# Kernel optimization log

Hardware: AMD Instinct MI355X
Metric: run time of the kernel (lower is better)

## Reference

```python
import jax, jax.numpy as jnp
import numpy as np


def setup_inputs() -> dict:
    key = jax.random.key(0)
    k1, k2, k3 = jax.random.split(key, 3)
    N, D, E = 100000, 128, 600000
    h = jax.random.normal(k1, (N, D), dtype=jnp.float32)
    src = jax.random.randint(k2, (E,), 0, N, dtype=jnp.int64)
    dst = jax.random.randint(k3, (E,), 0, N, dtype=jnp.int64)
    return {"h": h, "src": src, "dst": dst}


def reference(h, src, dst):
    # DGL fn.u_dot_v('h','h','out'): per-edge dot product of src/dst node
    # features, output shape (E, 1).
    hu = h[src]            # (E, D) gather of source-node features
    hv = h[dst]            # (E, D) gather of destination-node features
    out = jnp.sum(hu * hv, axis=-1, keepdims=True)  # (E, 1)
    return out
```

## Files before the change

kernel.cpp:

```cpp
#include <hip/hip_runtime.h>
#include <hip/hip_fp16.h>


constexpr int D   = 128;
constexpr int LPE = 16;
constexpr int UNR = 4;

__global__ __launch_bounds__(256) void convert_kernel(
    const float* __restrict__ h, __half* __restrict__ hh, int n4)
{
    const int stride = gridDim.x * blockDim.x;
    for (int k = blockIdx.x * blockDim.x + threadIdx.x; k < n4; k += stride) {
        float4 v = reinterpret_cast<const float4*>(h)[k];
        __half2 a = __floats2half2_rn(v.x, v.y);
        __half2 b = __floats2half2_rn(v.z, v.w);
        uint2 packed;
        packed.x = *reinterpret_cast<unsigned int*>(&a);
        packed.y = *reinterpret_cast<unsigned int*>(&b);
        reinterpret_cast<uint2*>(hh)[k] = packed;
    }
}

#if defined(__has_builtin) && __has_builtin(__builtin_amdgcn_fdot2)
#define HAS_FDOT2 1
#else
#define HAS_FDOT2 0
#endif

__device__ __forceinline__ float dot8(uint4 ua, uint4 ub)
{
    float acc = 0.f;
    const unsigned int* pa = &ua.x;
    const unsigned int* pb = &ub.x;
#pragma unroll
    for (int i = 0; i < 4; ++i) {
        __half2 ha = *reinterpret_cast<const __half2*>(&pa[i]);
        __half2 hb = *reinterpret_cast<const __half2*>(&pb[i]);
#if HAS_FDOT2
        acc = __builtin_amdgcn_fdot2(*reinterpret_cast<_Float16_2*>(&ha),
                                     *reinterpret_cast<_Float16_2*>(&hb),
                                     acc, false);
#else
        float2 fa = __half22float2(ha);
        float2 fb = __half22float2(hb);
        acc = fmaf(fa.x, fb.x, acc);
        acc = fmaf(fa.y, fb.y, acc);
#endif
    }
    return acc;
}

__device__ __forceinline__ float reduce16(float acc)
{
    acc += __shfl_xor(acc, 1);
    acc += __shfl_xor(acc, 2);
    acc += __shfl_xor(acc, 4);
    acc += __shfl_xor(acc, 8);
    return acc;
}

__global__ __launch_bounds__(256) void edge_dot_f16_kernel(
    const __half* __restrict__ hh,
    const int*    __restrict__ src,
    const int*    __restrict__ dst,
    float*        __restrict__ out,
    int E)
{
    const int tid    = blockIdx.x * blockDim.x + threadIdx.x;
    const int sub    = threadIdx.x & (LPE - 1);
    const int slot   = tid / LPE;
    const int nslots = (gridDim.x * blockDim.x) / LPE;
    const int step   = UNR * nslots;

    int e = slot;
    int s[UNR], t[UNR];
    if (e + (UNR - 1) * nslots < E) {
#pragma unroll
        for (int k = 0; k < UNR; ++k) {
            s[k] = src[e + k * nslots];
            t[k] = dst[e + k * nslots];
        }
    }

    while (e + (UNR - 1) * nslots < E) {
        uint4 a[UNR], b[UNR];
#pragma unroll
        for (int k = 0; k < UNR; ++k) {
            a[k] = *(reinterpret_cast<const uint4*>(hh + (size_t)s[k] * D) + sub);
            b[k] = *(reinterpret_cast<const uint4*>(hh + (size_t)t[k] * D) + sub);
        }

        const int en = e + step;
        if (en + (UNR - 1) * nslots < E) {
#pragma unroll
            for (int k = 0; k < UNR; ++k) {
                s[k] = src[en + k * nslots];
                t[k] = dst[en + k * nslots];
            }
        }

#pragma unroll
        for (int k = 0; k < UNR; ++k) {
            float acc = reduce16(dot8(a[k], b[k]));
            if (sub == 0) out[e + k * nslots] = acc;
        }
        e = en;
    }

    for (; e < E; e += nslots) {
        const int ss = src[e];
        const int tt = dst[e];
        uint4 a = *(reinterpret_cast<const uint4*>(hh + (size_t)ss * D) + sub);
        uint4 b = *(reinterpret_cast<const uint4*>(hh + (size_t)tt * D) + sub);
        float acc = reduce16(dot8(a, b));
        if (sub == 0) out[e] = acc;
    }
}

__global__ __launch_bounds__(256) void edge_dot_f32_kernel(
    const float* __restrict__ h,
    const int*   __restrict__ src,
    const int*   __restrict__ dst,
    float*       __restrict__ out,
    int E)
{
    const int tid    = blockIdx.x * blockDim.x + threadIdx.x;
    const int sub    = threadIdx.x & (LPE - 1);
    const int slot   = tid / LPE;
    const int nslots = (gridDim.x * blockDim.x) / LPE;
    const int off    = sub * 2;

    for (int e = slot; e < E; e += nslots) {
        const int s = src[e];
        const int t = dst[e];
        const float4* hu = reinterpret_cast<const float4*>(h + (size_t)s * D) + off;
        const float4* hv = reinterpret_cast<const float4*>(h + (size_t)t * D) + off;
        float4 a0 = hu[0]; float4 a1 = hu[1];
        float4 b0 = hv[0]; float4 b1 = hv[1];
        float acc = a0.x * b0.x + a0.y * b0.y + a0.z * b0.z + a0.w * b0.w
                  + a1.x * b1.x + a1.y * b1.y + a1.z * b1.z + a1.w * b1.w;
        acc = reduce16(acc);
        if (sub == 0) out[e] = acc;
    }
}

extern "C" void kernel_launch(void* const* d_in, const int* in_sizes, int n_in,
                              void* d_out, int out_size, void* d_ws, size_t ws_size,
                              hipStream_t stream) {
    const float* h   = (const float*)d_in[0];
    const int*   src = (const int*)d_in[1];
    const int*   dst = (const int*)d_in[2];
    float*       out = (float*)d_out;

    const int hN = in_sizes[0];
    const int E  = in_sizes[1];

    const int block = 256;
    int grid = (E + (block / LPE) - 1) / (block / LPE);
    if (grid > 2048) grid = 2048;

    const size_t need = (size_t)hN * sizeof(__half);
    if (ws_size >= need) {
        __half* hh = (__half*)d_ws;
        convert_kernel<<<2048, 256, 0, stream>>>(h, hh, hN / 4);
        edge_dot_f16_kernel<<<grid, block, 0, stream>>>(hh, src, dst, out, E);
    } else {
        edge_dot_f32_kernel<<<grid, block, 0, stream>>>(h, src, dst, out, E);
    }
}
```

Baseline: 131.3 us.

## Slice fp16 feature table by column and compute per-slice partial dots

Converts the fp32 node table into eight column slices of 16 halves each (3.2 MB per slice), so each pass over the edges touches a slice small enough to stay cache-resident. A partial-dot kernel computes per-slice partial dot products into a workspace buffer, and a third kernel sums the eight partials. This aims to turn random full-row gathers from DRAM into cache hits. The cost is re-reading the src/dst indices eight times, writing and reading 8×E floats of partials, and one extra kernel launch. The old unrolled edge loop is also simplified in the fallback path.

```diff
diff --git a/kernel.cpp b/kernel.cpp
--- a/kernel.cpp
+++ b/kernel.cpp
@@ -2,9 +2,142 @@
 #include <hip/hip_fp16.h>
 
 
-constexpr int D   = 128;
+constexpr int D      = 128;
+constexpr int NSLICE = 8;
+constexpr int SW     = 16;
+constexpr int CHUNKS = 256;
+
+#if defined(__has_builtin)
+#if __has_builtin(__builtin_amdgcn_fdot2)
+#define HAS_FDOT2 1
+#endif
+#endif
+#ifndef HAS_FDOT2
+#define HAS_FDOT2 0
+#endif
+
+__device__ __forceinline__ unsigned packh2(float x, float y) {
+    __half2 p = __floats2half2_rn(x, y);
+    return *reinterpret_cast<unsigned*>(&p);
+}
+
+__device__ __forceinline__ float fdot2acc(unsigned a, unsigned b, float acc) {
+    __half2 ha = *reinterpret_cast<__half2*>(&a);
+    __half2 hb = *reinterpret_cast<__half2*>(&b);
+#if HAS_FDOT2
+    return __builtin_amdgcn_fdot2(*reinterpret_cast<_Float16_2*>(&ha),
+                                  *reinterpret_cast<_Float16_2*>(&hb),
+                                  acc, false);
+#else
+    float2 fa = __half22float2(ha);
+    float2 fb = __half22float2(hb);
+    return fmaf(fa.y, fb.y, fmaf(fa.x, fb.x, acc));
+#endif
+}
+
+__device__ __forceinline__ float dot8u(uint4 a, uint4 b) {
+    float acc = 0.f;
+    acc = fdot2acc(a.x, b.x, acc);
+    acc = fdot2acc(a.y, b.y, acc);
+    acc = fdot2acc(a.z, b.z, acc);
+    acc = fdot2acc(a.w, b.w, acc);
+    return acc;
+}
+
+__global__ __launch_bounds__(256) void convert_slice_kernel(
+    const float* __restrict__ h, __half* __restrict__ hsl, int N)
+{
+    const int total  = N * NSLICE;
+    const int stride = gridDim.x * blockDim.x;
+    for (int task = blockIdx.x * blockDim.x + threadIdx.x; task < total; task += stride) {
+        const int n = task >> 3;
+        const int s = task & 7;
+        const float4* srow = reinterpret_cast<const float4*>(h + (size_t)n * D + s * SW);
+        float4 v0 = srow[0], v1 = srow[1], v2 = srow[2], v3 = srow[3];
+        uint4 w0, w1;
+        w0.x = packh2(v0.x, v0.y); w0.y = packh2(v0.z, v0.w);
+        w0.z = packh2(v1.x, v1.y); w0.w = packh2(v1.z, v1.w);
+        w1.x = packh2(v2.x, v2.y); w1.y = packh2(v2.z, v2.w);
+        w1.z = packh2(v3.x, v3.y); w1.w = packh2(v3.z, v3.w);
+        uint4* drow = reinterpret_cast<uint4*>(hsl + ((size_t)s * N + n) * SW);
+        drow[0] = w0;
+        drow[1] = w1;
+    }
+}
+
+__global__ __launch_bounds__(256) void partial_dot_kernel(
+    const __half* __restrict__ hsl,
+    const int*    __restrict__ src,
+    const int*    __restrict__ dst,
+    float*        __restrict__ partial,
+    int E, int N, int chunk)
+{
+    const int s = blockIdx.x & (NSLICE - 1);
+    const int c = blockIdx.x >> 3;
+    const __half* __restrict__ base = hsl + (size_t)s * N * SW;
+    float* __restrict__ pout = partial + (size_t)s * E;
+
+    const int start = c * chunk;
+    const int end   = (start + chunk < E) ? (start + chunk) : E;
+    const int lp    = threadIdx.x >> 1;
+    const int j     = threadIdx.x & 1;
+    const int PSTR  = 128;
+    const int joff  = j * 8;
+
+    int e = start + lp;
+    for (; e + PSTR < end; e += 2 * PSTR) {
+        const int e2 = e + PSTR;
+        const int s1 = src[e],  t1 = dst[e];
+        const int s2 = src[e2], t2 = dst[e2];
+        uint4 a1 = *reinterpret_cast<const uint4*>(base + (size_t)s1 * SW + joff);
+        uint4 b1 = *reinterpret_cast<const uint4*>(base + (size_t)t1 * SW + joff);
+        uint4 a2 = *reinterpret_cast<const uint4*>(base + (size_t)s2 * SW + joff);
+        uint4 b2 = *reinterpret_cast<const uint4*>(base + (size_t)t2 * SW + joff);
+        float d1 = dot8u(a1, b1);
+        float d2 = dot8u(a2, b2);
+        d1 += __shfl_xor(d1, 1);
+        d2 += __shfl_xor(d2, 1);
+        if (j == 0) {
+            pout[e]  = d1;
+            pout[e2] = d2;
+        }
+    }
+    for (; e < end; e += PSTR) {
+        const int s1 = src[e], t1 = dst[e];
+        uint4 a1 = *reinterpret_cast<const uint4*>(base + (size_t)s1 * SW + joff);
+        uint4 b1 = *reinterpret_cast<const uint4*>(base + (size_t)t1 * SW + joff);
+        float d1 = dot8u(a1, b1);
+        d1 += __shfl_xor(d1, 1);
+        if (j == 0) pout[e] = d1;
+    }
+}
+
+__global__ __launch_bounds__(256) void reduce8_kernel(
+    const float* __restrict__ partial, float* __restrict__ out, int E)
+{
+    const int stride = gridDim.x * blockDim.x;
+    if ((E & 3) == 0) {
+        const int n4 = E >> 2;
+        for (int i = blockIdx.x * blockDim.x + threadIdx.x; i < n4; i += stride) {
+            float4 acc = reinterpret_cast<const float4*>(partial)[i];
+#pragma unroll
+            for (int s = 1; s < NSLICE; ++s) {
+                float4 p = reinterpret_cast<const float4*>(partial + (size_t)s * E)[i];
+                acc.x += p.x; acc.y += p.y; acc.z += p.z; acc.w += p.w;
+            }
+            reinterpret_cast<float4*>(out)[i] = acc;
+        }
+    } else {
+        for (int i = blockIdx.x * blockDim.x + threadIdx.x; i < E; i += stride) {
+            float acc = 0.f;
+#pragma unroll
+            for (int s = 0; s < NSLICE; ++s) acc += partial[(size_t)s * E + i];
+            out[i] = acc;
+        }
+    }
+}
+
 constexpr int LPE = 16;
-constexpr int UNR = 4;
 
 __global__ __launch_bounds__(256) void convert_kernel(
     const float* __restrict__ h, __half* __restrict__ hh, int n4)
@@ -12,42 +145,11 @@
     const int stride = gridDim.x * blockDim.x;
     for (int k = blockIdx.x * blockDim.x + threadIdx.x; k < n4; k += stride) {
         float4 v = reinterpret_cast<const float4*>(h)[k];
-        __half2 a = __floats2half2_rn(v.x, v.y);
-        __half2 b = __floats2half2_rn(v.z, v.w);
         uint2 packed;
-        packed.x = *reinterpret_cast<unsigned int*>(&a);
-        packed.y = *reinterpret_cast<unsigned int*>(&b);
+        packed.x = packh2(v.x, v.y);
+        packed.y = packh2(v.z, v.w);
         reinterpret_cast<uint2*>(hh)[k] = packed;
     }
-}
-
-#if defined(__has_builtin) && __has_builtin(__builtin_amdgcn_fdot2)
-#define HAS_FDOT2 1
-#else
-#define HAS_FDOT2 0
-#endif
-
-__device__ __forceinline__ float dot8(uint4 ua, uint4 ub)
-{
-    float acc = 0.f;
-    const unsigned int* pa = &ua.x;
-    const unsigned int* pb = &ub.x;
-#pragma unroll
-    for (int i = 0; i < 4; ++i) {
-        __half2 ha = *reinterpret_cast<const __half2*>(&pa[i]);
-        __half2 hb = *reinterpret_cast<const __half2*>(&pb[i]);
-#if HAS_FDOT2
-        acc = __builtin_amdgcn_fdot2(*reinterpret_cast<_Float16_2*>(&ha),
-                                     *reinterpret_cast<_Float16_2*>(&hb),
-                                     acc, false);
-#else
-        float2 fa = __half22float2(ha);
-        float2 fb = __half22float2(hb);
-        acc = fmaf(fa.x, fb.x, acc);
-        acc = fmaf(fa.y, fb.y, acc);
-#endif
-    }
-    return acc;
 }
 
 __device__ __forceinline__ float reduce16(float acc)
@@ -70,49 +172,13 @@
     const int sub    = threadIdx.x & (LPE - 1);
     const int slot   = tid / LPE;
     const int nslots = (gridDim.x * blockDim.x) / LPE;
-    const int step   = UNR * nslots;
-
-    int e = slot;
-    int s[UNR], t[UNR];
-    if (e + (UNR - 1) * nslots < E) {
-#pragma unroll
-        for (int k = 0; k < UNR; ++k) {
-            s[k] = src[e + k * nslots];
-            t[k] = dst[e + k * nslots];
-        }
-    }
-
-    while (e + (UNR - 1) * nslots < E) {
-        uint4 a[UNR], b[UNR];
-#pragma unroll
-        for (int k = 0; k < UNR; ++k) {
-            a[k] = *(reinterpret_cast<const uint4*>(hh + (size_t)s[k] * D) + sub);
-            b[k] = *(reinterpret_cast<const uint4*>(hh + (size_t)t[k] * D) + sub);
-        }
-
-        const int en = e + step;
-        if (en + (UNR - 1) * nslots < E) {
-#pragma unroll
-            for (int k = 0; k < UNR; ++k) {
-                s[k] = src[en + k * nslots];
-                t[k] = dst[en + k * nslots];
-            }
-        }
-
-#pragma unroll
-        for (int k = 0; k < UNR; ++k) {
-            float acc = reduce16(dot8(a[k], b[k]));
-            if (sub == 0) out[e + k * nslots] = acc;
-        }
-        e = en;
-    }
-
-    for (; e < E; e += nslots) {
+
+    for (int e = slot; e < E; e += nslots) {
         const int ss = src[e];
         const int tt = dst[e];
         uint4 a = *(reinterpret_cast<const uint4*>(hh + (size_t)ss * D) + sub);
         uint4 b = *(reinterpret_cast<const uint4*>(hh + (size_t)tt * D) + sub);
-        float acc = reduce16(dot8(a, b));
+        float acc = reduce16(dot8u(a, b));
         if (sub == 0) out[e] = acc;
     }
 }
@@ -154,17 +220,29 @@
 
     const int hN = in_sizes[0];
     const int E  = in_sizes[1];
-
-    const int block = 256;
-    int grid = (E + (block / LPE) - 1) / (block / LPE);
-    if (grid > 2048) grid = 2048;
-
-    const size_t need = (size_t)hN * sizeof(__half);
-    if (ws_size >= need) {
+    const int N  = hN / D;
+
+    const size_t slabBytes = ((size_t)hN * sizeof(__half) + 15) & ~(size_t)15;
+    const size_t partBytes = (size_t)NSLICE * E * sizeof(float);
+
+    if (ws_size >= slabBytes + partBytes) {
+        __half* hsl     = (__half*)d_ws;
+        float*  partial = (float*)((char*)d_ws + slabBytes);
+
+        convert_slice_kernel<<<2048, 256, 0, stream>>>(h, hsl, N);
+        const int chunk = (E + CHUNKS - 1) / CHUNKS;
+        partial_dot_kernel<<<NSLICE * CHUNKS, 256, 0, stream>>>(
+            hsl, src, dst, partial, E, N, chunk);
+        reduce8_kernel<<<1024, 256, 0, stream>>>(partial, out, E);
+    } else if (ws_size >= (size_t)hN * sizeof(__half)) {
         __half* hh = (__half*)d_ws;
         convert_kernel<<<2048, 256, 0, stream>>>(h, hh, hN / 4);
-        edge_dot_f16_kernel<<<grid, block, 0, stream>>>(hh, src, dst, out, E);
+        int grid = (E + (256 / LPE) - 1) / (256 / LPE);
+        if (grid > 2048) grid = 2048;
+        edge_dot_f16_kernel<<<grid, 256, 0, stream>>>(hh, src, dst, out, E);
     } else {
-        edge_dot_f32_kernel<<<grid, block, 0, stream>>>(h, src, dst, out, E);
-    }
-}
+        int grid = (E + (256 / LPE) - 1) / (256 / LPE);
+        if (grid > 2048) grid = 2048;
+        edge_dot_f32_kernel<<<grid, 256, 0, stream>>>(h, src, dst, out, E);
+    }
+}
```

Result: slower. 143.5 us (+9.3%).
